# Performance work log

Measured on AMD Instinct MI355X. Metric: run time of the kernel, lower is better.

## Reference

```python
import math
import jax, jax.numpy as jnp
import numpy as np

B, T, HIDDEN = 2, 2048, 1024
H, HKV, D = 16, 16, 64


def _rope_tables(T, D):
    inv_freq = 1.0 / (10000.0 ** (jnp.arange(0, D, 2, dtype=jnp.float32) / D))
    t = jnp.arange(T, dtype=jnp.float32)
    freqs = jnp.outer(t, inv_freq)               # [T, D/2]
    emb = jnp.concatenate([freqs, freqs], axis=-1)  # [T, D]
    return jnp.cos(emb), jnp.sin(emb)


def setup_inputs() -> dict:
    key = jax.random.key(0)
    k1, k2, k3 = jax.random.split(key, 3)
    hidden_states = jax.random.normal(k1, (B, T, HIDDEN), dtype=jnp.float32)
    cos, sin = _rope_tables(T, D)
    # trunc-normal-ish init, std = 1/sqrt(fan_in)
    w_qkv = jax.random.normal(k2, ((H + 2 * HKV) * D, HIDDEN), dtype=jnp.float32) / math.sqrt(HIDDEN)
    w_o = jax.random.normal(k3, (HIDDEN, H * D), dtype=jnp.float32) / math.sqrt(H * D)
    return {"hidden_states": hidden_states, "cos": cos, "sin": sin, "w_qkv": w_qkv, "w_o": w_o}


def _rotate_half(x):
    x1, x2 = jnp.split(x, 2, axis=-1)
    return jnp.concatenate([-x2, x1], axis=-1)


def reference(hidden_states, cos, sin, w_qkv, w_o):
    b, t, _ = hidden_states.shape
    # fused QKV projection: [B,T,(H+2*HKV)*D]
    qkv = jnp.einsum('bti,oi->bto', hidden_states, w_qkv)
    qkv = qkv.reshape(b, t, H + 2 * HKV, D)
    q = qkv[:, :, :H]                    # [B,T,H,D]
    k = qkv[:, :, H:H + HKV]             # [B,T,HKV,D]
    v = qkv[:, :, H + HKV:]              # [B,T,HKV,D]
    # inline RoPE; cos/sin broadcast over heads
    c = cos[:, None, :]
    s = sin[:, None, :]
    q = q * c + _rotate_half(q) * s
    k = k * c + _rotate_half(k) * s
    scale = 1.0 / math.sqrt(D)
    attn_scores = jnp.einsum('bthd,bThd->bhtT', q, k) * scale  # [B,H,T,T]
    mask = jnp.tril(jnp.ones((t, t), dtype=bool))
    attn_scores = jnp.where(mask[None, None, :, :], attn_scores, -1e9)
    attn = jax.nn.softmax(attn_scores, axis=-1)
    context = jnp.einsum('bhtT,bThd->bthd', attn, v).reshape(b, t, H * D)
    return jnp.einsum('bti,oi->bto', context, w_o)
```

## Files before the change

kernel.cpp:

```cpp
#include <hip/hip_runtime.h>

typedef __bf16 bf16_t;
typedef __bf16 bf16x4 __attribute__((ext_vector_type(4)));
typedef __bf16 bf16x8 __attribute__((ext_vector_type(8)));
typedef float f32x4 __attribute__((ext_vector_type(4)));
typedef unsigned long long u64;

#define MFMA16(a, b, c) __builtin_amdgcn_mfma_f32_16x16x32_bf16((a), (b), (c), 0, 0, 0)

#define LDG2LDS16(g, l)                                                        \
    __builtin_amdgcn_global_load_lds(                                          \
        (const __attribute__((address_space(1))) void*)(g),                    \
        (__attribute__((address_space(3))) void*)(l), 16, 0, 0)

__device__ inline bf16x8 load8(const float* p) {
    const f32x4 a = *(const f32x4*)p;
    const f32x4 b = *(const f32x4*)(p + 4);
    bf16x8 r;
#pragma unroll
    for (int i = 0; i < 4; i++) { r[i] = (bf16_t)a[i]; r[4 + i] = (bf16_t)b[i]; }
    return r;
}

__device__ inline bf16x4 shfl4(bf16x4 v, int src) {
    u64 x;
    __builtin_memcpy(&x, &v, 8);
    x = __shfl(x, src, 64);
    bf16x4 r;
    __builtin_memcpy(&r, &x, 8);
    return r;
}

__global__ __launch_bounds__(256) void convert_kernel(const float* __restrict__ hs,
                                                      const float* __restrict__ wqkv,
                                                      const float* __restrict__ wo,
                                                      bf16_t* __restrict__ outb) {
    const size_t c = ((size_t)blockIdx.x * 256 + threadIdx.x) * 8;
    const float* src;
    size_t off;
    if (c < 4194304) { src = hs; off = c; }
    else if (c < 7340032) { src = wqkv; off = c - 4194304; }
    else { src = wo; off = c - 7340032; }
    *(bf16x8*)(outb + c) = load8(src + off);
}


template <int MODE, int NDIM, int BM>
__global__ __launch_bounds__(256) void gemm_bt(const bf16_t* __restrict__ A,
                                               const bf16_t* __restrict__ B,
                                               float* __restrict__ outp,
                                               bf16_t* __restrict__ q_ws,
                                               bf16_t* __restrict__ k_ws,
                                               bf16_t* __restrict__ v_ws,
                                               const float* __restrict__ cosb,
                                               const float* __restrict__ sinb) {
    constexpr int K = 1024;
    constexpr int IM = BM / 32;
    __shared__ __align__(16) bf16_t As[BM * 32];
    __shared__ __align__(16) bf16_t Bs[128 * 32];

    const int tid = threadIdx.x;
    const int w = tid >> 6;
    const int lane = tid & 63;
    const int lr = lane & 15;
    const int quad = lane >> 4;
    const int m0 = blockIdx.y * BM;
    const int n0 = blockIdx.x * 128;
    const int wm = (w & 1) * (BM / 2);
    const int wn = (w >> 1) * 64;

    const int srow = tid >> 2;
    const int skk = (tid & 3) * 8;
    const bf16_t* gA0 = A + (size_t)(m0 + srow) * K + skk;
    const bf16_t* gA1 = gA0 + (size_t)64 * K;
    const bf16_t* gB0 = B + (size_t)(n0 + srow) * K + skk;
    const bf16_t* gB1 = gB0 + (size_t)64 * K;
    bf16_t* lA0 = As + w * 512;
    bf16_t* lA1 = As + 2048 + w * 512;
    bf16_t* lB0 = Bs + w * 512;
    bf16_t* lB1 = Bs + 2048 + w * 512;

    f32x4 acc[IM][4] = {};

    for (int k0 = 0; k0 < K; k0 += 32) {
        LDG2LDS16(gA0 + k0, lA0);
        if constexpr (BM == 128) LDG2LDS16(gA1 + k0, lA1);
        LDG2LDS16(gB0 + k0, lB0);
        LDG2LDS16(gB1 + k0, lB1);
        __syncthreads();

        bf16x8 af[IM], bfm[4];
#pragma unroll
        for (int im = 0; im < IM; im++)
            af[im] = *(const bf16x8*)&As[(wm + im * 16 + lr) * 32 + quad * 8];
#pragma unroll
        for (int in = 0; in < 4; in++)
            bfm[in] = *(const bf16x8*)&Bs[(wn + in * 16 + lr) * 32 + quad * 8];
#pragma unroll
        for (int im = 0; im < IM; im++)
#pragma unroll
            for (int in = 0; in < 4; in++)
                acc[im][in] = MFMA16(af[im], bfm[in], acc[im][in]);
        __syncthreads();
    }

    if constexpr (MODE == 0) {
#pragma unroll
        for (int im = 0; im < IM; im++)
#pragma unroll
            for (int in = 0; in < 4; in++)
#pragma unroll
                for (int r = 0; r < 4; r++) {
                    const int m = m0 + wm + im * 16 + quad * 4 + r;
                    const int n = n0 + wn + in * 16 + lr;
                    outp[(size_t)m * NDIM + n] = acc[im][in][r];
                }
    } else {
        const int j = (n0 + wn) >> 6;
        if (j < 32) {
            const bool isq = (j < 16);
            const float qs = 0.125f * 1.44269504089f;
#pragma unroll
            for (int im = 0; im < IM; im++) {
#pragma unroll
                for (int r = 0; r < 4; r++) {
                    const int m = m0 + wm + im * 16 + quad * 4 + r;
                    const int b = m >> 11;
                    const int t = m & 2047;
#pragma unroll
                    for (int in = 0; in < 2; in++) {
                        const int d = in * 16 + lr;
                        const float x1 = acc[im][in][r];
                        const float x2 = acc[im][in + 2][r];
                        const float c = cosb[t * 64 + d];
                        const float s = sinb[t * 64 + d];
                        float y1 = x1 * c - x2 * s;
                        float y2 = x2 * c + x1 * s;
                        if (isq) {
                            y1 *= qs; y2 *= qs;
                            const size_t base =
                                ((size_t)(b * 16 + j) * 2048 + t) * 64 + d;
                            q_ws[base] = (bf16_t)y1;
                            q_ws[base + 32] = (bf16_t)y2;
                        } else {
                            const int bh = b * 16 + (j - 16);
                            const size_t off =
                                ((size_t)(bh * 128 + (t >> 4)) * 2) * 512 +
                                ((t & 15) + (d >> 3) * 16) * 8 + (d & 7);
                            k_ws[off] = (bf16_t)y1;
                            k_ws[off + 512] = (bf16_t)y2;
                        }
                    }
                }
            }
        } else {
#pragma unroll
            for (int im = 0; im < IM; im++)
#pragma unroll
                for (int in = 0; in < 4; in++)
#pragma unroll
                    for (int r = 0; r < 4; r++) {
                        const int m = m0 + wm + im * 16 + quad * 4 + r;
                        const int b = m >> 11;
                        const int t = m & 2047;
                        const int d = in * 16 + lr;
                        const int bh = b * 16 + (j - 32);
                        const size_t off =
                            ((size_t)(bh * 64 + (t >> 5)) * 4 + (d >> 4)) * 512 +
                            ((d & 15) + ((t & 31) >> 3) * 16) * 8 + (t & 7);
                        v_ws[off] = (bf16_t)acc[im][in][r];
                    }
        }
    }
}

__global__ __launch_bounds__(256) void attn_kernel(const bf16_t* __restrict__ q_ws,
                                                   const bf16_t* __restrict__ k_ws,
                                                   const bf16_t* __restrict__ v_ws,
                                                   bf16_t* __restrict__ ctx) {
    const int tid = threadIdx.x;
    const int w = tid >> 6;
    const int lane = tid & 63;
    const int lr = lane & 15;
    const int quad = lane >> 4;
    const int bh = blockIdx.x & 31;
    const int qt = 31 - (blockIdx.x >> 5);
    const int trow = qt * 64 + w * 16;
    const int query = trow + lr;

    const bf16_t* qb = q_ws + ((size_t)bh * 2048 + trow + lr) * 64 + quad * 8;
    const bf16x8 qlo = *(const bf16x8*)qb;
    const bf16x8 qhi = *(const bf16x8*)(qb + 32);

    const bf16_t* kbase = k_ws + (size_t)bh * 131072 + lane * 8;
    const bf16_t* vbase = v_ws + (size_t)bh * 131072 + lane * 8;

    f32x4 o[4] = {};
    float lrun = 0.0f;

    const int srcLow = ((quad & 1) << 5) + lr;
    const int srcHigh = srcLow + 16;
    const bool loSel = (quad < 2);

    bf16x8 kc[8];
#pragma unroll
    for (int n = 0; n < 4; n++) {
        kc[2 * n] = *(const bf16x8*)(kbase + (size_t)(n * 2) * 512);
        kc[2 * n + 1] = *(const bf16x8*)(kbase + (size_t)(n * 2 + 1) * 512);
    }

    for (int kb = 0; kb <= qt; kb++) {
        bf16x8 vv[2][4];
#pragma unroll
        for (int hh = 0; hh < 2; hh++)
#pragma unroll
            for (int n = 0; n < 4; n++)
                vv[hh][n] = *(const bf16x8*)(vbase +
                    (size_t)((kb * 2 + hh) * 4 + n) * 512);

        const int kbn = (kb < qt) ? kb + 1 : kb;
        bf16x8 kn[8];
#pragma unroll
        for (int n = 0; n < 4; n++) {
            kn[2 * n] = *(const bf16x8*)(kbase + (size_t)((kbn * 4 + n) * 2) * 512);
            kn[2 * n + 1] = *(const bf16x8*)(kbase + (size_t)((kbn * 4 + n) * 2 + 1) * 512);
        }

        const int u0 = kb * 64;
        f32x4 s[4];
#pragma unroll
        for (int n = 0; n < 4; n++) {
            const f32x4 z = {};
            s[n] = MFMA16(kc[2 * n], qlo, z);
            s[n] = MFMA16(kc[2 * n + 1], qhi, s[n]);
        }

        if (kb == qt) {
#pragma unroll
            for (int n = 0; n < 4; n++)
#pragma unroll
                for (int r = 0; r < 4; r++)
                    if (u0 + n * 16 + quad * 4 + r > query) s[n][r] = -1e9f;
        }

        f32x4 p[4];
#pragma unroll
        for (int n = 0; n < 4; n++)
#pragma unroll
            for (int r = 0; r < 4; r++) p[n][r] = exp2f(s[n][r]);

        lrun += ((p[0][0] + p[0][1]) + (p[0][2] + p[0][3])) +
                ((p[1][0] + p[1][1]) + (p[1][2] + p[1][3])) +
                ((p[2][0] + p[2][1]) + (p[2][2] + p[2][3])) +
                ((p[3][0] + p[3][1]) + (p[3][2] + p[3][3]));

        bf16x4 pb[4];
#pragma unroll
        for (int n = 0; n < 4; n++)
#pragma unroll
            for (int r = 0; r < 4; r++) pb[n][r] = (bf16_t)p[n][r];

#pragma unroll
        for (int hh = 0; hh < 2; hh++) {
            const bf16x4 a0 = shfl4(pb[2 * hh], srcLow);
            const bf16x4 a1 = shfl4(pb[2 * hh + 1], srcLow);
            const bf16x4 b0 = shfl4(pb[2 * hh], srcHigh);
            const bf16x4 b1 = shfl4(pb[2 * hh + 1], srcHigh);
            const bf16x4 lo = loSel ? a0 : a1;
            const bf16x4 hi = loSel ? b0 : b1;
            bf16x8 pf;
#pragma unroll
            for (int r = 0; r < 4; r++) { pf[r] = lo[r]; pf[4 + r] = hi[r]; }

#pragma unroll
            for (int n = 0; n < 4; n++)
                o[n] = MFMA16(vv[hh][n], pf, o[n]);
        }

#pragma unroll
        for (int i = 0; i < 8; i++) kc[i] = kn[i];
    }

    lrun += __shfl_xor(lrun, 16);
    lrun += __shfl_xor(lrun, 32);

    const int b = bh >> 4;
    const int hd = bh & 15;
    const float inv = 1.0f / fmaxf(lrun, 1e-30f);
    const size_t base = ((size_t)b * 2048 + query) * 1024 + hd * 64 + quad * 4;
#pragma unroll
    for (int n = 0; n < 4; n++) {
        bf16x4 ob;
#pragma unroll
        for (int r = 0; r < 4; r++) ob[r] = (bf16_t)(o[n][r] * inv);
        *(bf16x4*)&ctx[base + n * 16] = ob;
    }
}

extern "C" void kernel_launch(void* const* d_in, const int* in_sizes, int n_in,
                              void* d_out, int out_size, void* d_ws, size_t ws_size,
                              hipStream_t stream) {
    const float* hs = (const float*)d_in[0];
    const float* cosb = (const float*)d_in[1];
    const float* sinb = (const float*)d_in[2];
    const float* wqkv = (const float*)d_in[3];
    const float* wo = (const float*)d_in[4];
    float* out = (float*)d_out;

    char* ws = (char*)d_ws;
    bf16_t* hs_b = (bf16_t*)(ws);
    bf16_t* wqkv_b = hs_b + 4194304;
    bf16_t* wo_b = hs_b + 7340032;
    bf16_t* q_ws = (bf16_t*)(ws + (size_t)(16u << 20));
    bf16_t* k_ws = (bf16_t*)(ws + (size_t)(24u << 20));
    bf16_t* v_ws = (bf16_t*)(ws + (size_t)(32u << 20));
    bf16_t* ctx = (bf16_t*)(ws);

    const dim3 blk(256);

    convert_kernel<<<dim3(4096), blk, 0, stream>>>(hs, wqkv, wo, hs_b);

    gemm_bt<1, 3072, 128><<<dim3(24, 32), blk, 0, stream>>>(
        hs_b, wqkv_b, nullptr, q_ws, k_ws, v_ws, cosb, sinb);

    attn_kernel<<<dim3(1024), blk, 0, stream>>>(q_ws, k_ws, v_ws, ctx);

    gemm_bt<0, 1024, 64><<<dim3(8, 64), blk, 0, stream>>>(
        ctx, wo_b, out, nullptr, nullptr, nullptr, nullptr, nullptr);
}
```

Measured before the change: 181.1 us.

## Pair causal query tiles per block and use permlane swaps for P

Each attention block now handles two query tiles, pr and 31-pr, so every block does the same amount of causal work and the grid halves to 512 blocks. The P-matrix relayout switches from ds_bpermute shuffles to permlane16/32 swap builtins when the compiler provides them. exp2f is replaced with the raw hardware exp2 builtin. The risks are lower occupancy and parallelism from the smaller grid, and the two tiles in each block run one after the other.

```diff
diff --git a/kernel.cpp b/kernel.cpp
--- a/kernel.cpp
+++ b/kernel.cpp
@@ -4,6 +4,7 @@
 typedef __bf16 bf16x4 __attribute__((ext_vector_type(4)));
 typedef __bf16 bf16x8 __attribute__((ext_vector_type(8)));
 typedef float f32x4 __attribute__((ext_vector_type(4)));
+typedef unsigned int u32x2 __attribute__((ext_vector_type(2)));
 typedef unsigned long long u64;
 
 #define MFMA16(a, b, c) __builtin_amdgcn_mfma_f32_16x16x32_bf16((a), (b), (c), 0, 0, 0)
@@ -13,12 +14,24 @@
         (const __attribute__((address_space(1))) void*)(g),                    \
         (__attribute__((address_space(3))) void*)(l), 16, 0, 0)
 
+#if __has_builtin(__builtin_amdgcn_exp2f)
+#define EXP2(x) __builtin_amdgcn_exp2f(x)
+#else
+#define EXP2(x) exp2f(x)
+#endif
+
 __device__ inline bf16x8 load8(const float* p) {
     const f32x4 a = *(const f32x4*)p;
     const f32x4 b = *(const f32x4*)(p + 4);
     bf16x8 r;
 #pragma unroll
     for (int i = 0; i < 4; i++) { r[i] = (bf16_t)a[i]; r[4 + i] = (bf16_t)b[i]; }
+    return r;
+}
+
+__device__ inline u32x2 as2(bf16x4 v) {
+    u32x2 r;
+    __builtin_memcpy(&r, &v, 8);
     return r;
 }
 
@@ -174,6 +187,107 @@
     }
 }
 
+__device__ inline void flash_tile(int qt, int quad, int lr, int query,
+                                  const bf16_t* __restrict__ kbase,
+                                  const bf16_t* __restrict__ vbase,
+                                  bf16x8 qlo, bf16x8 qhi,
+                                  f32x4* o, float& lrun) {
+    bf16x8 kc[8];
+#pragma unroll
+    for (int n = 0; n < 4; n++) {
+        kc[2 * n] = *(const bf16x8*)(kbase + (size_t)(n * 2) * 512);
+        kc[2 * n + 1] = *(const bf16x8*)(kbase + (size_t)(n * 2 + 1) * 512);
+    }
+
+    for (int kb = 0; kb <= qt; kb++) {
+        bf16x8 vv[2][4];
+#pragma unroll
+        for (int hh = 0; hh < 2; hh++)
+#pragma unroll
+            for (int n = 0; n < 4; n++)
+                vv[hh][n] = *(const bf16x8*)(vbase +
+                    (size_t)((kb * 2 + hh) * 4 + n) * 512);
+
+        const int kbn = (kb < qt) ? kb + 1 : kb;
+        bf16x8 kn[8];
+#pragma unroll
+        for (int n = 0; n < 4; n++) {
+            kn[2 * n] = *(const bf16x8*)(kbase + (size_t)((kbn * 4 + n) * 2) * 512);
+            kn[2 * n + 1] = *(const bf16x8*)(kbase + (size_t)((kbn * 4 + n) * 2 + 1) * 512);
+        }
+
+        const int u0 = kb * 64;
+        f32x4 s[4];
+#pragma unroll
+        for (int n = 0; n < 4; n++) {
+            const f32x4 z = {};
+            s[n] = MFMA16(kc[2 * n], qlo, z);
+            s[n] = MFMA16(kc[2 * n + 1], qhi, s[n]);
+        }
+
+        if (kb == qt) {
+#pragma unroll
+            for (int n = 0; n < 4; n++)
+#pragma unroll
+                for (int r = 0; r < 4; r++)
+                    if (u0 + n * 16 + quad * 4 + r > query) s[n][r] = -1e9f;
+        }
+
+        f32x4 p[4];
+#pragma unroll
+        for (int n = 0; n < 4; n++)
+#pragma unroll
+            for (int r = 0; r < 4; r++) p[n][r] = EXP2(s[n][r]);
+
+        lrun += ((p[0][0] + p[0][1]) + (p[0][2] + p[0][3])) +
+                ((p[1][0] + p[1][1]) + (p[1][2] + p[1][3])) +
+                ((p[2][0] + p[2][1]) + (p[2][2] + p[2][3])) +
+                ((p[3][0] + p[3][1]) + (p[3][2] + p[3][3]));
+
+        bf16x4 pb[4];
+#pragma unroll
+        for (int n = 0; n < 4; n++)
+#pragma unroll
+            for (int r = 0; r < 4; r++) pb[n][r] = (bf16_t)p[n][r];
+
+#pragma unroll
+        for (int hh = 0; hh < 2; hh++) {
+            bf16x8 pf;
+#if __has_builtin(__builtin_amdgcn_permlane16_swap) && \
+    __has_builtin(__builtin_amdgcn_permlane32_swap)
+            const u32x2 P0 = as2(pb[2 * hh]);
+            const u32x2 P1 = as2(pb[2 * hh + 1]);
+            const u32x2 s1a = __builtin_amdgcn_permlane16_swap(P0[0], P0[1], false, false);
+            const u32x2 s1b = __builtin_amdgcn_permlane16_swap(P1[0], P1[1], false, false);
+            const u32x2 s2a = __builtin_amdgcn_permlane32_swap(s1a[0], s1b[0], false, false);
+            const u32x2 s2b = __builtin_amdgcn_permlane32_swap(s1a[1], s1b[1], false, false);
+            const u32x2 s3a = __builtin_amdgcn_permlane16_swap(s2a[0], s2a[1], false, false);
+            const u32x2 s3b = __builtin_amdgcn_permlane16_swap(s2b[0], s2b[1], false, false);
+            const unsigned pfd[4] = {s3a[0], s3a[1], s3b[0], s3b[1]};
+            __builtin_memcpy(&pf, pfd, 16);
+#else
+            const int srcLow = ((quad & 1) << 5) + lr;
+            const int srcHigh = srcLow + 16;
+            const bool loSel = (quad < 2);
+            const bf16x4 a0 = shfl4(pb[2 * hh], srcLow);
+            const bf16x4 a1 = shfl4(pb[2 * hh + 1], srcLow);
+            const bf16x4 b0 = shfl4(pb[2 * hh], srcHigh);
+            const bf16x4 b1 = shfl4(pb[2 * hh + 1], srcHigh);
+            const bf16x4 lo = loSel ? a0 : a1;
+            const bf16x4 hi = loSel ? b0 : b1;
+#pragma unroll
+            for (int r = 0; r < 4; r++) { pf[r] = lo[r]; pf[4 + r] = hi[r]; }
+#endif
+#pragma unroll
+            for (int n = 0; n < 4; n++)
+                o[n] = MFMA16(vv[hh][n], pf, o[n]);
+        }
+
+#pragma unroll
+        for (int i = 0; i < 8; i++) kc[i] = kn[i];
+    }
+}
+
 __global__ __launch_bounds__(256) void attn_kernel(const bf16_t* __restrict__ q_ws,
                                                    const bf16_t* __restrict__ k_ws,
                                                    const bf16_t* __restrict__ v_ws,
@@ -184,116 +298,39 @@
     const int lr = lane & 15;
     const int quad = lane >> 4;
     const int bh = blockIdx.x & 31;
-    const int qt = 31 - (blockIdx.x >> 5);
-    const int trow = qt * 64 + w * 16;
-    const int query = trow + lr;
-
-    const bf16_t* qb = q_ws + ((size_t)bh * 2048 + trow + lr) * 64 + quad * 8;
-    const bf16x8 qlo = *(const bf16x8*)qb;
-    const bf16x8 qhi = *(const bf16x8*)(qb + 32);
+    const int pr = blockIdx.x >> 5;
+    const int b = bh >> 4;
+    const int hd = bh & 15;
 
     const bf16_t* kbase = k_ws + (size_t)bh * 131072 + lane * 8;
     const bf16_t* vbase = v_ws + (size_t)bh * 131072 + lane * 8;
 
-    f32x4 o[4] = {};
-    float lrun = 0.0f;
-
-    const int srcLow = ((quad & 1) << 5) + lr;
-    const int srcHigh = srcLow + 16;
-    const bool loSel = (quad < 2);
-
-    bf16x8 kc[8];
-#pragma unroll
-    for (int n = 0; n < 4; n++) {
-        kc[2 * n] = *(const bf16x8*)(kbase + (size_t)(n * 2) * 512);
-        kc[2 * n + 1] = *(const bf16x8*)(kbase + (size_t)(n * 2 + 1) * 512);
-    }
-
-    for (int kb = 0; kb <= qt; kb++) {
-        bf16x8 vv[2][4];
-#pragma unroll
-        for (int hh = 0; hh < 2; hh++)
-#pragma unroll
-            for (int n = 0; n < 4; n++)
-                vv[hh][n] = *(const bf16x8*)(vbase +
-                    (size_t)((kb * 2 + hh) * 4 + n) * 512);
-
-        const int kbn = (kb < qt) ? kb + 1 : kb;
-        bf16x8 kn[8];
+#pragma unroll
+    for (int half = 0; half < 2; half++) {
+        const int qt = half ? (31 - pr) : pr;
+        const int trow = qt * 64 + w * 16;
+        const int query = trow + lr;
+
+        const bf16_t* qb = q_ws + ((size_t)bh * 2048 + trow + lr) * 64 + quad * 8;
+        const bf16x8 qlo = *(const bf16x8*)qb;
+        const bf16x8 qhi = *(const bf16x8*)(qb + 32);
+
+        f32x4 o[4] = {};
+        float lrun = 0.0f;
+        flash_tile(qt, quad, lr, query, kbase, vbase, qlo, qhi, o, lrun);
+
+        lrun += __shfl_xor(lrun, 16);
+        lrun += __shfl_xor(lrun, 32);
+
+        const float inv = 1.0f / fmaxf(lrun, 1e-30f);
+        const size_t base = ((size_t)b * 2048 + query) * 1024 + hd * 64 + quad * 4;
 #pragma unroll
         for (int n = 0; n < 4; n++) {
-            kn[2 * n] = *(const bf16x8*)(kbase + (size_t)((kbn * 4 + n) * 2) * 512);
-            kn[2 * n + 1] = *(const bf16x8*)(kbase + (size_t)((kbn * 4 + n) * 2 + 1) * 512);
-        }
-
-        const int u0 = kb * 64;
-        f32x4 s[4];
-#pragma unroll
-        for (int n = 0; n < 4; n++) {
-            const f32x4 z = {};
-            s[n] = MFMA16(kc[2 * n], qlo, z);
-            s[n] = MFMA16(kc[2 * n + 1], qhi, s[n]);
-        }
-
-        if (kb == qt) {
-#pragma unroll
-            for (int n = 0; n < 4; n++)
-#pragma unroll
-                for (int r = 0; r < 4; r++)
-                    if (u0 + n * 16 + quad * 4 + r > query) s[n][r] = -1e9f;
-        }
-
-        f32x4 p[4];
-#pragma unroll
-        for (int n = 0; n < 4; n++)
-#pragma unroll
-            for (int r = 0; r < 4; r++) p[n][r] = exp2f(s[n][r]);
-
-        lrun += ((p[0][0] + p[0][1]) + (p[0][2] + p[0][3])) +
-                ((p[1][0] + p[1][1]) + (p[1][2] + p[1][3])) +
-                ((p[2][0] + p[2][1]) + (p[2][2] + p[2][3])) +
-                ((p[3][0] + p[3][1]) + (p[3][2] + p[3][3]));
-
-        bf16x4 pb[4];
-#pragma unroll
-        for (int n = 0; n < 4; n++)
-#pragma unroll
-            for (int r = 0; r < 4; r++) pb[n][r] = (bf16_t)p[n][r];
-
-#pragma unroll
-        for (int hh = 0; hh < 2; hh++) {
-            const bf16x4 a0 = shfl4(pb[2 * hh], srcLow);
-            const bf16x4 a1 = shfl4(pb[2 * hh + 1], srcLow);
-            const bf16x4 b0 = shfl4(pb[2 * hh], srcHigh);
-            const bf16x4 b1 = shfl4(pb[2 * hh + 1], srcHigh);
-            const bf16x4 lo = loSel ? a0 : a1;
-            const bf16x4 hi = loSel ? b0 : b1;
-            bf16x8 pf;
-#pragma unroll
-            for (int r = 0; r < 4; r++) { pf[r] = lo[r]; pf[4 + r] = hi[r]; }
-
-#pragma unroll
-            for (int n = 0; n < 4; n++)
-                o[n] = MFMA16(vv[hh][n], pf, o[n]);
-        }
-
-#pragma unroll
-        for (int i = 0; i < 8; i++) kc[i] = kn[i];
-    }
-
-    lrun += __shfl_xor(lrun, 16);
-    lrun += __shfl_xor(lrun, 32);
-
-    const int b = bh >> 4;
-    const int hd = bh & 15;
-    const float inv = 1.0f / fmaxf(lrun, 1e-30f);
-    const size_t base = ((size_t)b * 2048 + query) * 1024 + hd * 64 + quad * 4;
-#pragma unroll
-    for (int n = 0; n < 4; n++) {
-        bf16x4 ob;
-#pragma unroll
-        for (int r = 0; r < 4; r++) ob[r] = (bf16_t)(o[n][r] * inv);
-        *(bf16x4*)&ctx[base + n * 16] = ob;
+            bf16x4 ob;
+#pragma unroll
+            for (int r = 0; r < 4; r++) ob[r] = (bf16_t)(o[n][r] * inv);
+            *(bf16x4*)&ctx[base + n * 16] = ob;
+        }
     }
 }
 
@@ -323,7 +360,7 @@
     gemm_bt<1, 3072, 128><<<dim3(24, 32), blk, 0, stream>>>(
         hs_b, wqkv_b, nullptr, q_ws, k_ws, v_ws, cosb, sinb);
 
-    attn_kernel<<<dim3(1024), blk, 0, stream>>>(q_ws, k_ws, v_ws, ctx);
+    attn_kernel<<<dim3(512), blk, 0, stream>>>(q_ws, k_ws, v_ws, ctx);
 
     gemm_bt<0, 1024, 64><<<dim3(8, 64), blk, 0, stream>>>(
         ctx, wo_b, out, nullptr, nullptr, nullptr, nullptr, nullptr);
```

After: 178.0 us. About the same (-1.7%).
